# Kernel tuning notes

Measured on AMD Instinct MI355X. Metric: run time of the kernel, lower is better.

Reference implementation:

```python
import jax, jax.numpy as jnp
import numpy as np

PATCH = 3          # patch size for SSD cost
PAD = PATCH // 2
K_NN = 8           # number of NN candidates kept per pixel
N_ITERS = 10       # PatchMatch iterations (forward default n_iters=10)
_DY = jnp.array([d // PATCH for d in range(PATCH * PATCH)], dtype=jnp.int32)
_DX = jnp.array([d % PATCH for d in range(PATCH * PATCH)], dtype=jnp.int32)


def _patches(x):
    # x: [C,H,W] -> [C, P*P, H, W] edge-padded patch neighborhoods
    C, H, W = x.shape
    xp = jnp.pad(x, ((0, 0), (PAD, PAD), (PAD, PAD)), mode='edge')
    return jnp.stack([xp[:, dy:dy + H, dx:dx + W]
                      for dy in range(PATCH) for dx in range(PATCH)], axis=1)


def _cost(a_pat, b_pad, s):
    # a_pat: [C,P2,H,W]; b_pad: [C,H+2p,W+2p]; s: [2,H,W] int -> SSD cost [H,W]
    iy = s[0][None] + _DY[:, None, None]   # [P2,H,W]
    ix = s[1][None] + _DX[:, None, None]
    b_g = b_pad[:, iy, ix]                 # [C,P2,H,W] gathered target patches
    return jnp.sum((a_pat - b_g) ** 2, axis=(0, 1))


def patchmatch_search(a, b, key, k=K_NN, n_iters=N_ITERS):
    # a, b: [C,H,W]. Returns shifts [k,2,H,W] int32 and costs [k,H,W].
    C, H, W = a.shape
    a_pat = _patches(a)
    b_pad = jnp.pad(b, ((0, 0), (PAD, PAD), (PAD, PAD)), mode='edge')
    cost1 = lambda s: _cost(a_pat, b_pad, s)
    hi = jnp.array([H, W], dtype=jnp.int32).reshape(1, 2, 1, 1)
    dx1 = jnp.array([0, 1], jnp.int32).reshape(1, 2, 1, 1)
    dy1 = jnp.array([1, 0], jnp.int32).reshape(1, 2, 1, 1)
    k0, key = jax.random.split(key)
    shifts = jax.random.randint(k0, (k, 2, H, W), 0, hi)
    costs = jax.lax.map(cost1, shifts)
    radii = [max(W // 2, 1), max(W // 8, 1), max(W // 32, 1), 1]

    def step(carry, it):
        shifts, costs = carry
        kk = jax.random.fold_in(key, it)
        # parallel propagation of neighbors' shifts
        left = jnp.roll(shifts, 1, axis=3) + dx1
        right = jnp.roll(shifts, -1, axis=3) - dx1
        up = jnp.roll(shifts, 1, axis=2) + dy1
        down = jnp.roll(shifts, -1, axis=2) - dy1
        # random search with shrinking radii
        rand_c = [shifts + jax.random.randint(jax.random.fold_in(kk, i),
                                              shifts.shape, -r, r + 1)
                  for i, r in enumerate(radii)]
        cands = jnp.concatenate([left, right, up, down] + rand_c, axis=0)
        cands = jnp.clip(cands, 0, hi - 1)
        new_costs = jax.lax.map(cost1, cands)
        all_s = jnp.concatenate([shifts, cands], axis=0)      # [M,2,H,W]
        all_c = jnp.concatenate([costs, new_costs], axis=0)   # [M,H,W]
        neg_top, idx = jax.lax.top_k(-jnp.moveaxis(all_c, 0, -1), k)  # [H,W,k]
        s_hw = jnp.transpose(all_s, (2, 3, 0, 1))             # [H,W,M,2]
        sel = jnp.take_along_axis(s_hw, idx[..., None], axis=2)  # [H,W,k,2]
        return (jnp.transpose(sel, (2, 3, 0, 1)), jnp.moveaxis(-neg_top, -1, 0)), None

    (shifts, costs), _ = jax.lax.scan(step, (shifts, costs), jnp.arange(n_iters))
    return shifts, costs


def setup_inputs() -> dict:
    key = jax.random.key(0)
    kq, kk, kv = jax.random.split(key, 3)
    q = jax.random.normal(kq, (1, 32, 128, 128), jnp.float32)
    k = jax.random.normal(kk, (1, 32, 128, 128), jnp.float32)
    v = jax.random.normal(kv, (4, 64, 128, 128), jnp.float32)
    return {"q": q, "k": k, "v": v}


def reference(q, k, v):
    # PatchMatch k-NN search between q[0] and k[0]
    shifts, costs = patchmatch_search(q[0], k[0], jax.random.key(42))
    w = jax.nn.softmax(-costs, axis=0)                 # [K,H,W]
    g = v[:, :, shifts[:, 0], shifts[:, 1]]            # [B,Cv,K,H,W] gather
    return jnp.sum(w[None, None] * g, axis=2)          # [B,Cv,H,W]
```

## Files before the change

### kernel.cpp

```cpp
#include <hip/hip_runtime.h>
#include <cstdint>

#define NPIX 16384
#define KNN 8
#define PW 130
#define NPPAD (PW * PW)
#define NPH 8

typedef float f32x4 __attribute__((ext_vector_type(4)));

#define FENCE asm volatile("" ::: "memory");

__host__ __device__ __forceinline__ void tf2x32(uint32_t k0, uint32_t k1,
                                                uint32_t x0, uint32_t x1,
                                                uint32_t& o0, uint32_t& o1) {
  uint32_t ks2 = k0 ^ k1 ^ 0x1BD11BDAu;
  x0 += k0; x1 += k1;
#define TFR(r) { x0 += x1; x1 = (x1 << r) | (x1 >> (32 - r)); x1 ^= x0; }
  TFR(13) TFR(15) TFR(26) TFR(6)  x0 += k1;  x1 += ks2 + 1u;
  TFR(17) TFR(29) TFR(16) TFR(24) x0 += ks2; x1 += k0 + 2u;
  TFR(13) TFR(15) TFR(26) TFR(6)  x0 += k0;  x1 += k1 + 3u;
  TFR(17) TFR(29) TFR(16) TFR(24) x0 += k1;  x1 += ks2 + 4u;
  TFR(13) TFR(15) TFR(26) TFR(6)  x0 += ks2; x1 += k0 + 5u;
#undef TFR
  o0 = x0; o1 = x1;
}

__device__ __forceinline__ uint32_t rbits32(uint32_t ka, uint32_t kb, uint32_t j) {
  uint32_t o0, o1;
  tf2x32(ka, kb, 0u, j, o0, o1);
  return o0 ^ o1;
}

__device__ __forceinline__ int rnd_int(uint4 K, uint32_t j, uint32_t span,
                                       uint32_t mult, int minv) {
  uint32_t hi = rbits32(K.x, K.y, j);
  uint32_t lo = rbits32(K.z, K.w, j);
  uint32_t off = ((hi % span) * mult + (lo % span)) % span;
  return minv + (int)off;
}

__device__ __forceinline__ float cost_eval_pl(const float* __restrict__ apt,
                                              const float* __restrict__ bpt,
                                              int py0, int px0, int sy, int sx) {
  float acc = 0.f;
#pragma unroll
  for (int ph = 0; ph < NPH; ++ph) {
    const float* ab = apt + ((size_t)ph * NPPAD + (size_t)(py0 * PW + px0)) * 4;
    const float* bb = bpt + ((size_t)ph * NPPAD + (size_t)(sy * PW + sx)) * 4;
    f32x4 av[9], bv[9];
#pragma unroll
    for (int p = 0; p < 9; ++p) {
      int dy = p / 3, dx = p - dy * 3;
      av[p] = *(const f32x4*)(ab + (dy * PW + dx) * 4);
      bv[p] = *(const f32x4*)(bb + (dy * PW + dx) * 4);
    }
#pragma unroll
    for (int j = 0; j < 4; ++j) {
#pragma unroll
      for (int p = 0; p < 9; ++p) {
        float d = __fsub_rn(av[p][j], bv[p][j]);
        acc = __fadd_rn(acc, __fmul_rn(d, d));
      }
    }
  }
  return acc;
}

__global__ __launch_bounds__(256) void pad_kernel(
    const float* __restrict__ a, const float* __restrict__ b,
    float* __restrict__ apt, float* __restrict__ bpt) {
  int t = (int)(blockIdx.x * blockDim.x + threadIdx.x);
  if (t >= 32 * NPPAD) return;
  int lo = t & 3;
  int rest = t >> 2;
  int pos = rest % NPPAD;
  int ph = rest / NPPAD;
  int c = ph * 4 + lo;
  int py = pos / PW, px = pos % PW;
  int y = py - 1; y = y < 0 ? 0 : (y > 127 ? 127 : y);
  int x = px - 1; x = x < 0 ? 0 : (x > 127 ? 127 : x);
  int src = (c << 14) + (y << 7) + x;
  apt[t] = a[src];
  bpt[t] = b[src];
}

__global__ __launch_bounds__(256) void init_kernel(
    const float* __restrict__ apt, const float* __restrict__ bpt,
    uint32_t* __restrict__ npack, float* __restrict__ ncost, uint4 IK) {
  int t = (int)(blockIdx.x * blockDim.x + threadIdx.x);
  int pix = t & (NPIX - 1);
  int s = t >> 14;
  int py0 = pix >> 7, px0 = pix & 127;
  uint32_t j0 = (uint32_t)(s * 2) * 16384u + (uint32_t)pix;
  int sy = rnd_int(IK, j0, 128u, 0u, 0);
  int sx = rnd_int(IK, j0 + 16384u, 128u, 0u, 0);
  float cst = cost_eval_pl(apt, bpt, py0, px0, sy, sx);
  npack[t] = (uint32_t)((sy << 7) | sx);
  ncost[t] = cst;
}

__global__ __launch_bounds__(64, 4) void step_kernel(
    const float* __restrict__ apt, const float* __restrict__ bpt,
    const uint32_t* __restrict__ ppack, const float* __restrict__ pcost,
    uint32_t* __restrict__ npack, float* __restrict__ ncost,
    uint4 K0, uint4 K1, uint4 K2, uint4 K3) {
  __shared__ f32x4 lds[576];
  int bidx = (int)blockIdx.x;
  int pix = ((bidx & 7) << 11) | (bidx >> 3);
  int lane = (int)threadIdx.x;
  int py0 = pix >> 7, px0 = pix & 127;
  int g = lane >> 3, s = lane & 7;

  uint32_t old_pack = 0u; float old_cost_f = 0.f;
  if (lane < 8) {
    old_pack = ppack[lane * NPIX + pix];
    old_cost_f = pcost[lane * NPIX + pix];
  }

  int sy, sx;
  if (g < 4) {
    int nh = py0, nw = px0, dsy = 0, dsx = 0;
    if (g == 0)      { nw = (px0 + 127) & 127; dsx = 1;  }
    else if (g == 1) { nw = (px0 + 1) & 127;   dsx = -1; }
    else if (g == 2) { nh = (py0 + 127) & 127; dsy = 1;  }
    else             { nh = (py0 + 1) & 127;   dsy = -1; }
    uint32_t p = ppack[s * NPIX + (nh << 7) + nw];
    sy = (int)(p >> 7) + dsy;
    sx = (int)(p & 127u) + dsx;
  } else {
    uint32_t p = ppack[s * NPIX + pix];
    uint4 Ki      = (g == 4) ? K0   : (g == 5) ? K1  : (g == 6) ? K2 : K3;
    uint32_t span = (g == 4) ? 129u : (g == 5) ? 33u : (g == 6) ? 9u : 3u;
    uint32_t mult = (g == 4) ? 16u  : (g == 5) ? 4u  : (g == 6) ? 4u : 1u;
    int minv      = (g == 4) ? -64  : (g == 5) ? -16 : (g == 6) ? -4 : -1;
    uint32_t j0 = (uint32_t)(s * 2) * 16384u + (uint32_t)pix;
    sy = (int)(p >> 7)   + rnd_int(Ki, j0, span, mult, minv);
    sx = (int)(p & 127u) + rnd_int(Ki, j0 + 16384u, span, mult, minv);
  }
  sy = sy < 0 ? 0 : (sy > 127 ? 127 : sy);
  sx = sx < 0 ? 0 : (sx > 127 ? 127 : sx);
  uint32_t cnd_pack = (uint32_t)((sy << 7) | sx);

  int base_[9];
#pragma unroll
  for (int i = 0; i < 9; ++i) {
    int f = i * 64 + lane;
    int c = f / 9, p = f - c * 9;
    int dy = p / 3, dx = p - dy * 3;
    uint32_t pk = (uint32_t)__shfl((int)cnd_pack, c);
    int py = (int)(pk >> 7) + dy;
    int px = (int)(pk & 127u) + dx;
    base_[i] = (py * PW + px) * 4;
  }

  float acc = 0.f;
  f32x4 sA[9], sB[9];

#define STAGE_LOAD(BUF, PH)                                                 \
  _Pragma("unroll")                                                         \
  for (int i = 0; i < 9; ++i) {                                             \
    BUF[i] = *(const f32x4*)(bpt + (size_t)(PH) * (NPPAD * 4) + base_[i]);  \
  }

#define STAGE_WRITE(BUF)                                                    \
  _Pragma("unroll")                                                         \
  for (int i = 0; i < 9; ++i) {                                             \
    lds[i * 64 + lane] = BUF[i];                                            \
  }

#define EVAL(PH)                                                            \
  {                                                                         \
    const float* ab = apt + (size_t)(PH) * (NPPAD * 4)                      \
                     + (size_t)(py0 * PW + px0) * 4;                        \
    f32x4 av[9], bv[9];                                                     \
    _Pragma("unroll")                                                       \
    for (int p = 0; p < 9; ++p) {                                           \
      int dy = p / 3, dx = p - dy * 3;                                      \
      bv[p] = lds[lane * 9 + p];                                            \
      av[p] = *(const f32x4*)(ab + (dy * PW + dx) * 4);                     \
    }                                                                       \
    _Pragma("unroll")                                                       \
    for (int j = 0; j < 4; ++j) {                                           \
      _Pragma("unroll")                                                     \
      for (int p = 0; p < 9; ++p) {                                         \
        float d = __fsub_rn(av[p][j], bv[p][j]);                            \
        acc = __fadd_rn(acc, __fmul_rn(d, d));                              \
      }                                                                     \
    }                                                                       \
  }

  STAGE_LOAD(sA, 0)
  STAGE_LOAD(sB, 1)
  FENCE STAGE_WRITE(sA) STAGE_LOAD(sA, 2) FENCE EVAL(0)
  FENCE STAGE_WRITE(sB) STAGE_LOAD(sB, 3) FENCE EVAL(1)
  FENCE STAGE_WRITE(sA) STAGE_LOAD(sA, 4) FENCE EVAL(2)
  FENCE STAGE_WRITE(sB) STAGE_LOAD(sB, 5) FENCE EVAL(3)
  FENCE STAGE_WRITE(sA) STAGE_LOAD(sA, 6) FENCE EVAL(4)
  FENCE STAGE_WRITE(sB) STAGE_LOAD(sB, 7) FENCE EVAL(5)
  FENCE STAGE_WRITE(sA) FENCE EVAL(6)
  FENCE STAGE_WRITE(sB) FENCE EVAL(7)
#undef STAGE_LOAD
#undef STAGE_WRITE
#undef EVAL

  float cnd_cost = acc;

  unsigned long long new_key =
      ((unsigned long long)__float_as_uint(cnd_cost) << 32) | (unsigned)(8 + lane);
  unsigned long long old_key = (lane < 8)
      ? (((unsigned long long)__float_as_uint(old_cost_f) << 32) | (unsigned)lane)
      : ~0ull;
  bool new_used = false, old_used = (lane >= 8);

  uint32_t out_pack = 0u; float out_cost = 0.f;
#define TOPK_ROUND(R)                                                      \
  {                                                                        \
    unsigned long long kmin = new_used ? ~0ull : new_key;                  \
    if (!old_used && old_key < kmin) kmin = old_key;                       \
    _Pragma("unroll")                                                      \
    for (int off = 32; off; off >>= 1) {                                   \
      unsigned long long o = __shfl_xor(kmin, off);                        \
      if (o < kmin) kmin = o;                                              \
    }                                                                      \
    if (!new_used && new_key == kmin) new_used = true;                     \
    else if (!old_used && old_key == kmin) old_used = true;                \
    uint32_t idx = (uint32_t)kmin;                                         \
    float cst = __uint_as_float((uint32_t)(kmin >> 32));                   \
    int srcOld = (idx < 8u) ? (int)idx : 0;                                \
    int srcNew = (idx >= 8u) ? (int)(idx - 8u) : 0;                        \
    uint32_t po = __shfl(old_pack, srcOld);                                \
    uint32_t pn = __shfl(cnd_pack, srcNew);                                \
    uint32_t pk = (idx < 8u) ? po : pn;                                    \
    if (lane == R) { out_pack = pk; out_cost = cst; }                      \
  }
  TOPK_ROUND(0) TOPK_ROUND(1) TOPK_ROUND(2) TOPK_ROUND(3)
  TOPK_ROUND(4) TOPK_ROUND(5) TOPK_ROUND(6) TOPK_ROUND(7)
#undef TOPK_ROUND

  if (lane < 8) {
    npack[lane * NPIX + pix] = out_pack;
    ncost[lane * NPIX + pix] = out_cost;
  }
}

__global__ __launch_bounds__(256) void weights_kernel(
    const float* __restrict__ cost0, float* __restrict__ wbuf) {
  int pix = (int)(blockIdx.x * blockDim.x + threadIdx.x);
  if (pix >= NPIX) return;
  float c[KNN];
  float m = 3.4e38f;
#pragma unroll
  for (int s = 0; s < KNN; ++s) { c[s] = cost0[s * NPIX + pix]; m = fminf(m, c[s]); }
  float e[KNN]; float sum = 0.f;
#pragma unroll
  for (int s = 0; s < KNN; ++s) { e[s] = expf(m - c[s]); sum += e[s]; }
  float inv = 1.f / sum;
#pragma unroll
  for (int s = 0; s < KNN; ++s) wbuf[s * NPIX + pix] = e[s] * inv;
}

__global__ __launch_bounds__(256) void out_kernel(
    const float* __restrict__ v, const uint32_t* __restrict__ pack0,
    const float* __restrict__ wbuf, float* __restrict__ out) {
  int t = (int)(blockIdx.x * blockDim.x + threadIdx.x);
  int pix = t & (NPIX - 1);
  int ch = t >> 14;
  const float* vc = v + ((size_t)ch << 14);
  float acc = 0.f;
#pragma unroll
  for (int s = 0; s < KNN; ++s) {
    uint32_t p = pack0[s * NPIX + pix];
    float wgt = wbuf[s * NPIX + pix];
    acc = fmaf(wgt, vc[p], acc);
  }
  out[t] = acc;
}

static void h_split_fl(uint32_t ka, uint32_t kb, uint32_t o[4]) {
  tf2x32(ka, kb, 0u, 0u, o[0], o[1]);
  tf2x32(ka, kb, 0u, 1u, o[2], o[3]);
}

extern "C" void kernel_launch(void* const* d_in, const int* in_sizes, int n_in,
                              void* d_out, int out_size, void* d_ws, size_t ws_size,
                              hipStream_t stream) {
  const float* q = (const float*)d_in[0];
  const float* k = (const float*)d_in[1];
  const float* v = (const float*)d_in[2];
  float* out = (float*)d_out;

  uint32_t* ws = (uint32_t*)d_ws;
  uint32_t* pk[2] = { ws, ws + (size_t)KNN * NPIX };
  float* ct[2] = { (float*)(ws + (size_t)2 * KNN * NPIX),
                   (float*)(ws + (size_t)3 * KNN * NPIX) };
  float* wbuf = (float*)(ws + (size_t)4 * KNN * NPIX);
  float* apt  = (float*)(ws + (size_t)5 * KNN * NPIX);
  float* bpt  = apt + (size_t)32 * NPPAD;

  uint32_t sp[4];
  h_split_fl(0u, 42u, sp);
  uint32_t k0a = sp[0], k0b = sp[1];
  uint32_t kMa = sp[2], kMb = sp[3];

  pad_kernel<<<(32 * NPPAD + 255) / 256, 256, 0, stream>>>(q, k, apt, bpt);

  uint32_t ik[4];
  h_split_fl(k0a, k0b, ik);
  init_kernel<<<(KNN * NPIX) / 256, 256, 0, stream>>>(apt, bpt, pk[0], ct[0],
                                        make_uint4(ik[0], ik[1], ik[2], ik[3]));

  for (int it = 0; it < 10; ++it) {
    uint32_t ka, kb;
    tf2x32(kMa, kMb, 0u, (uint32_t)it, ka, kb);
    uint4 K[4];
    for (int i = 0; i < 4; ++i) {
      uint32_t ia, ib;
      tf2x32(ka, kb, 0u, (uint32_t)i, ia, ib);
      uint32_t o[4];
      h_split_fl(ia, ib, o);
      K[i] = make_uint4(o[0], o[1], o[2], o[3]);
    }
    step_kernel<<<NPIX, 64, 0, stream>>>(apt, bpt, pk[it & 1], ct[it & 1],
                                         pk[(it + 1) & 1], ct[(it + 1) & 1],
                                         K[0], K[1], K[2], K[3]);
  }

  weights_kernel<<<NPIX / 256, 256, 0, stream>>>(ct[0], wbuf);
  out_kernel<<<(4 * 64 * NPIX) / 256, 256, 0, stream>>>(v, pk[0], wbuf, out);
}
```

Before: 927.4 us.

## Stage candidate and query patches via direct global-to-LDS loads with double buffering

```diff
diff --git a/kernel.cpp b/kernel.cpp
--- a/kernel.cpp
+++ b/kernel.cpp
@@ -8,8 +8,8 @@
 #define NPH 8
 
 typedef float f32x4 __attribute__((ext_vector_type(4)));
-
-#define FENCE asm volatile("" ::: "memory");
+typedef __attribute__((address_space(3))) uint32_t lds_u32_t;
+typedef const __attribute__((address_space(1))) uint32_t glob_u32_t;
 
 __host__ __device__ __forceinline__ void tf2x32(uint32_t k0, uint32_t k1,
                                                 uint32_t x0, uint32_t x1,
@@ -105,7 +105,8 @@
     const uint32_t* __restrict__ ppack, const float* __restrict__ pcost,
     uint32_t* __restrict__ npack, float* __restrict__ ncost,
     uint4 K0, uint4 K1, uint4 K2, uint4 K3) {
-  __shared__ f32x4 lds[576];
+  __shared__ f32x4 ldsb[2][576];
+  __shared__ f32x4 ldsa[72];
   int bidx = (int)blockIdx.x;
   int pix = ((bidx & 7) << 11) | (bidx >> 3);
   int lane = (int)threadIdx.x;
@@ -154,32 +155,47 @@
     base_[i] = (py * PW + px) * 4;
   }
 
-  float acc = 0.f;
-  f32x4 sA[9], sB[9];
-
-#define STAGE_LOAD(BUF, PH)                                                 \
+  {
+    int q = lane;
+    int ph = q / 9, pos = q - ph * 9;
+    int dy = pos / 3, dx = pos - dy * 3;
+    const float* gp = apt + (size_t)ph * (NPPAD * 4)
+                     + (size_t)((py0 + dy) * PW + (px0 + dx)) * 4;
+    __builtin_amdgcn_global_load_lds((glob_u32_t*)gp, (lds_u32_t*)&ldsa[0], 16, 0, 0);
+  }
+  if (lane < 8) {
+    int q = 64 + lane;
+    int ph = q / 9, pos = q - ph * 9;
+    int dy = pos / 3, dx = pos - dy * 3;
+    const float* gp = apt + (size_t)ph * (NPPAD * 4)
+                     + (size_t)((py0 + dy) * PW + (px0 + dx)) * 4;
+    __builtin_amdgcn_global_load_lds((glob_u32_t*)gp, (lds_u32_t*)&ldsa[64], 16, 0, 0);
+  }
+
+#define GLB(BUF, PH)                                                        \
   _Pragma("unroll")                                                         \
   for (int i = 0; i < 9; ++i) {                                             \
-    BUF[i] = *(const f32x4*)(bpt + (size_t)(PH) * (NPPAD * 4) + base_[i]);  \
-  }
-
-#define STAGE_WRITE(BUF)                                                    \
-  _Pragma("unroll")                                                         \
-  for (int i = 0; i < 9; ++i) {                                             \
-    lds[i * 64 + lane] = BUF[i];                                            \
-  }
-
-#define EVAL(PH)                                                            \
+    __builtin_amdgcn_global_load_lds(                                       \
+        (glob_u32_t*)(bpt + (size_t)(PH) * (NPPAD * 4) + base_[i]),         \
+        (lds_u32_t*)&ldsb[BUF][i * 64], 16, 0, 0);                          \
+  }
+
+  GLB(0, 0)
+  GLB(1, 1)
+
+  float acc = 0.f;
+
+#define PHASE(PH, BUF, VMN, DOGL)                                           \
+  asm volatile("s_waitcnt vmcnt(" VMN ")" ::: "memory");                    \
   {                                                                         \
-    const float* ab = apt + (size_t)(PH) * (NPPAD * 4)                      \
-                     + (size_t)(py0 * PW + px0) * 4;                        \
     f32x4 av[9], bv[9];                                                     \
     _Pragma("unroll")                                                       \
     for (int p = 0; p < 9; ++p) {                                           \
-      int dy = p / 3, dx = p - dy * 3;                                      \
-      bv[p] = lds[lane * 9 + p];                                            \
-      av[p] = *(const f32x4*)(ab + (dy * PW + dx) * 4);                     \
+      bv[p] = ldsb[BUF][lane * 9 + p];                                      \
+      av[p] = ldsa[(PH) * 9 + p];                                           \
     }                                                                       \
+    asm volatile("s_waitcnt lgkmcnt(0)" ::: "memory");                      \
+    DOGL                                                                    \
     _Pragma("unroll")                                                       \
     for (int j = 0; j < 4; ++j) {                                           \
       _Pragma("unroll")                                                     \
@@ -190,19 +206,16 @@
     }                                                                       \
   }
 
-  STAGE_LOAD(sA, 0)
-  STAGE_LOAD(sB, 1)
-  FENCE STAGE_WRITE(sA) STAGE_LOAD(sA, 2) FENCE EVAL(0)
-  FENCE STAGE_WRITE(sB) STAGE_LOAD(sB, 3) FENCE EVAL(1)
-  FENCE STAGE_WRITE(sA) STAGE_LOAD(sA, 4) FENCE EVAL(2)
-  FENCE STAGE_WRITE(sB) STAGE_LOAD(sB, 5) FENCE EVAL(3)
-  FENCE STAGE_WRITE(sA) STAGE_LOAD(sA, 6) FENCE EVAL(4)
-  FENCE STAGE_WRITE(sB) STAGE_LOAD(sB, 7) FENCE EVAL(5)
-  FENCE STAGE_WRITE(sA) FENCE EVAL(6)
-  FENCE STAGE_WRITE(sB) FENCE EVAL(7)
-#undef STAGE_LOAD
-#undef STAGE_WRITE
-#undef EVAL
+  PHASE(0, 0, "9", GLB(0, 2))
+  PHASE(1, 1, "9", GLB(1, 3))
+  PHASE(2, 0, "9", GLB(0, 4))
+  PHASE(3, 1, "9", GLB(1, 5))
+  PHASE(4, 0, "9", GLB(0, 6))
+  PHASE(5, 1, "9", GLB(1, 7))
+  PHASE(6, 0, "9", )
+  PHASE(7, 1, "0", )
+#undef PHASE
+#undef GLB
 
   float cnd_cost = acc;
 
```

After: 972.0 us. 1.05x slower.
